# Kernel tuning notes

Measured on AMD Instinct MI355X. Metric: run time of the kernel, lower is better.

Reference implementation:

```python
import jax, jax.numpy as jnp
import numpy as np
from jax.scipy.special import gammaln, logsumexp

NEG = -1e9  # finite large-negative to keep gradients NaN-free


def setup_inputs() -> dict:
    key = jax.random.key(0)
    ks = jax.random.split(key, 8)
    B, T, D, C, K = 8, 4096, 64, 32, 20
    features = jax.random.normal(ks[0], (B, T, D), dtype=jnp.float32)
    # valid lengths in [T//2, T] so every sequence is long relative to K
    lengths = jax.random.randint(ks[1], (B,), T // 2, T + 1)
    poisson_log_rates = jax.random.normal(ks[2], (C,), dtype=jnp.float32) * 0.1 + jnp.log(8.0)
    gaussian_means = jax.random.normal(ks[3], (C, D), dtype=jnp.float32) * 0.5
    # tied diagonal covariance (as produced by initialize_gaussian / tied_diag)
    gaussian_cov = jnp.diag(jax.random.uniform(ks[4], (D,), minval=0.5, maxval=1.5))
    transition_logits = jax.random.normal(ks[5], (C, C), dtype=jnp.float32) * 0.1
    init_logits = jax.random.uniform(ks[6], (C,), dtype=jnp.float32)
    return dict(features=features, poisson_log_rates=poisson_log_rates,
                gaussian_means=gaussian_means, gaussian_cov=gaussian_cov,
                transition_logits=transition_logits, init_logits=init_logits,
                lengths=lengths, max_k=K)


def reference(features, poisson_log_rates, gaussian_means, gaussian_cov,
              transition_logits, init_logits, lengths, max_k):
    B, T, D = features.shape
    C = gaussian_means.shape[0]
    K = int(max_k)

    # ---- emission log-probs: tied full-covariance Gaussian per class -> (B,T,C)
    prec = jnp.linalg.inv(gaussian_cov)
    _, logdet = jnp.linalg.slogdet(gaussian_cov)
    xP = features @ prec                                        # (B,T,D)
    quad = jnp.einsum('btd,btd->bt', xP, features)              # x^T P x
    cross = jnp.einsum('btd,cd->btc', xP, gaussian_means)       # x^T P mu
    muPmu = jnp.einsum('cd,de,ce->c', gaussian_means, prec, gaussian_means)
    const = D * jnp.log(2.0 * jnp.pi) + logdet
    emit = -0.5 * (quad[:, :, None] - 2.0 * cross + muPmu[None, None, :] + const)  # (B,T,C)

    # ---- Poisson duration scores for d = 1..K -> (K,C)
    d = jnp.arange(1, K + 1, dtype=jnp.float32)[:, None]
    length_scores = d * poisson_log_rates[None, :] - jnp.exp(poisson_log_rates)[None, :] - gammaln(d + 1.0)

    # ---- normalized transition (to <- from, softmax over 'to' axis) and init
    trans = jax.nn.log_softmax(transition_logits, axis=0)       # trans[to, from]
    init = jax.nn.log_softmax(init_logits)

    # ---- span emission sums via cumsum differences (== sliding_sum windows)
    cum = jnp.concatenate([jnp.zeros((B, 1, C), emit.dtype), jnp.cumsum(emit, axis=1)], axis=1)  # (B,T+1,C)
    t_idx = jnp.arange(1, T + 1)[:, None]                        # (T,1) span end (exclusive)
    d_idx = jnp.arange(1, K + 1)[None, :]                        # (1,K) duration
    start = jnp.clip(t_idx - d_idx, 0, None)                     # (T,K) span start
    span = cum[:, t_idx, :] - cum[:, start, :]                   # (B,T,K,C)
    seg = span + length_scores[None, None, :, :]                 # add duration scores
    seg = jnp.transpose(seg, (1, 2, 0, 3))                       # (T,K,B,C)
    dur_valid = (d_idx <= t_idx)                                 # (T,K): need d <= t
    seg = jnp.where(dur_valid[:, :, None, None], seg, NEG)

    # ---- semi-Markov forward recursion over time.
    # buf[i] = alpha_star[t-1-i]; alpha_star[s][c] = best-sum of paths ending a
    # segment at s, already including the transition into the next label c.
    buf0 = jnp.full((K, B, C), NEG, emit.dtype).at[0].set(jnp.broadcast_to(init, (B, C)))

    def step(buf, seg_t):
        alpha_t = logsumexp(buf + seg_t, axis=0)                               # (B,C)
        astar = logsumexp(alpha_t[:, None, :] + trans[None, :, :], axis=2)     # (B,C)
        buf = jnp.concatenate([astar[None], buf[:-1]], axis=0)
        return buf, alpha_t

    _, alphas = jax.lax.scan(step, buf0, seg)                    # (T,B,C)
    logZ = logsumexp(alphas[lengths - 1, jnp.arange(B), :], axis=-1)
    return -logZ  # negative log marginal likelihood per sequence
```

## Files before the change

### kernel.cpp

```cpp
#include <hip/hip_runtime.h>
#include <math.h>

#define TT 4096
#define DD 64
#define CC 32
#define KK 20
#define TP 4112
#define NEGV -1.0e9f
#define L2E 1.44269504088896340736f
#define LN2f 0.69314718055994530942f

#if __has_builtin(__builtin_amdgcn_permlane32_swap)
#define HAVE_PLSWAP 1
#endif
#if __has_builtin(__builtin_amdgcn_permlane16_swap)
#define HAVE_PL16 1
#endif

__device__ __align__(16) float g_pmu[32 * 64];
__device__ __align__(16) float g_p2[64];
__device__ __align__(16) float g_mc[32];
__device__ __align__(16) float g_ls2[20 * 32];
__device__ __align__(16) float g_T[32 * 32];
__device__ __align__(16) float g_init2[32];
__device__ float g_cum[8 * TT * CC];
__device__ __align__(16) float g_cumT[8 * 32 * TP];

__device__ __forceinline__ float fexp2(float x) {
#if __has_builtin(__builtin_amdgcn_exp2f)
    return __builtin_amdgcn_exp2f(x);
#else
    return __exp2f(x);
#endif
}
__device__ __forceinline__ float flog2(float x) {
#if __has_builtin(__builtin_amdgcn_logf)
    return __builtin_amdgcn_logf(x);
#else
    return __log2f(x);
#endif
}

#define RF(x) __int_as_float(__builtin_amdgcn_readfirstlane(__float_as_int(x)))

__device__ __forceinline__ float xswap32(float x) {
#ifdef HAVE_PLSWAP
    int xi = __float_as_int(x);
    auto pr = __builtin_amdgcn_permlane32_swap(xi, xi, false, false);
    int r0 = ((const int*)&pr)[0];
    int r1 = ((const int*)&pr)[1];
    return (r0 == xi) ? __int_as_float(r1) : __int_as_float(r0);
#else
    return __shfl_xor(x, 32);
#endif
}

__device__ __forceinline__ float xswap16(float x) {
#ifdef HAVE_PL16
    int xi = __float_as_int(x);
    auto pr = __builtin_amdgcn_permlane16_swap(xi, xi, false, false);
    int r0 = ((const int*)&pr)[0];
    int r1 = ((const int*)&pr)[1];
    return (r0 == xi) ? __int_as_float(r1) : __int_as_float(r0);
#else
    return __shfl_xor(x, 16);
#endif
}

#define DPPF(dst, src, CTRL) \
    dst = __int_as_float(__builtin_amdgcn_update_dpp(0, __float_as_int(src), (CTRL), 0xF, 0xF, 1))

__global__ void smm_setup(const float* __restrict__ plr,
                          const float* __restrict__ mu,
                          const float* __restrict__ cov,
                          const float* __restrict__ tl,
                          const float* __restrict__ il) {
    int l = threadIdx.x;
    __shared__ float red[64];
    __shared__ float constc_s;
    float cd = cov[l * 64 + l];
    float pd = 1.0f / cd;
    red[l] = logf(cd);
    __syncthreads();
    if (l == 0) {
        float s = 0.f;
        for (int i = 0; i < 64; ++i) s += red[i];
        constc_s = 64.0f * logf(2.0f * 3.14159265358979323846f) + s;
    }
    __syncthreads();
    float constc = constc_s;

    g_p2[l] = 0.5f * L2E * pd;
    for (int c2 = 0; c2 < 32; ++c2)
        g_pmu[c2 * 64 + l] = L2E * pd * mu[c2 * 64 + l];

    if (l < 32) {
        float s = 0.f;
        for (int d2 = 0; d2 < 64; ++d2) {
            float m_ = mu[l * 64 + d2];
            s += m_ * m_ / cov[d2 * 64 + d2];
        }
        g_mc[l] = -0.5f * L2E * (s + constc);
    }
    for (int idx = l; idx < KK * CC; idx += 64) {
        int k = idx >> 5, c2 = idx & 31;
        float lr = plr[c2];
        g_ls2[idx] = L2E * ((float)(k + 1) * lr - expf(lr) - lgammaf((float)(k + 2)));
    }
    if (l < 32) {
        int from = l;
        float mx = -1e30f;
        for (int to = 0; to < 32; ++to) mx = fmaxf(mx, tl[to * 32 + from]);
        float s = 0.f;
        for (int to = 0; to < 32; ++to) s += expf(tl[to * 32 + from] - mx);
        float inv = 1.0f / s;
        for (int to = 0; to < 32; ++to)
            g_T[to * 32 + from] = expf(tl[to * 32 + from] - mx) * inv;
    }
    if (l == 32) {
        float mx = -1e30f;
        for (int c2 = 0; c2 < 32; ++c2) mx = fmaxf(mx, il[c2]);
        float s = 0.f;
        for (int c2 = 0; c2 < 32; ++c2) s += expf(il[c2] - mx);
        float lse = mx + logf(s);
        for (int c2 = 0; c2 < 32; ++c2) g_init2[c2] = L2E * (il[c2] - lse);
    }
}

__global__ __launch_bounds__(256) void smm_emit(const float* __restrict__ feat) {
    int tid = threadIdx.x;
    int c = tid & 31, tl_ = tid >> 5;
    int t = blockIdx.x * 8 + tl_;
    int b = blockIdx.y;
    const float4* x4 = (const float4*)(feat + ((size_t)b * TT + t) * DD);
    const float4* pm4 = (const float4*)(g_pmu + c * 64);
    const float4* p24 = (const float4*)g_p2;
    float acc = g_mc[c];
#pragma unroll
    for (int i = 0; i < 16; ++i) {
        float4 xv = x4[i], pm = pm4[i], pv = p24[i];
        acc = fmaf(pm.x, xv.x, acc); acc = fmaf(-pv.x * xv.x, xv.x, acc);
        acc = fmaf(pm.y, xv.y, acc); acc = fmaf(-pv.y * xv.y, xv.y, acc);
        acc = fmaf(pm.z, xv.z, acc); acc = fmaf(-pv.z * xv.z, xv.z, acc);
        acc = fmaf(pm.w, xv.w, acc); acc = fmaf(-pv.w * xv.w, xv.w, acc);
    }
    g_cum[((size_t)b * TT + t) * CC + c] = acc;
}

__global__ __launch_bounds__(256) void smm_scan() {
    int b = blockIdx.x;
    int tid = threadIdx.x;
    int c = tid & 31, g = tid >> 5;
    float* base = g_cum + (size_t)b * TT * CC + c;
    float* outT = g_cumT + ((size_t)b * 32 + c) * TP;
    int t0 = g * 512;
    float run = 0.f;
    for (int t = t0; t < t0 + 512; t += 8) {
        float v[8];
#pragma unroll
        for (int j = 0; j < 8; ++j) v[j] = base[(size_t)(t + j) * CC];
#pragma unroll
        for (int j = 0; j < 8; ++j) { run += v[j]; base[(size_t)(t + j) * CC] = run; }
    }
    __shared__ float tot[8][32];
    tot[g][c] = run;
    __syncthreads();
    float pre = 0.f;
#pragma unroll
    for (int gg = 0; gg < 7; ++gg) if (gg < g) pre += tot[gg][c];
    for (int t = t0; t < t0 + 512; t += 8) {
        float v[8];
#pragma unroll
        for (int j = 0; j < 8; ++j) v[j] = base[(size_t)(t + j) * CC] + pre;
        float4 w0, w1;
        w0.x = v[0]; w0.y = v[1]; w0.z = v[2]; w0.w = v[3];
        w1.x = v[4]; w1.y = v[5]; w1.z = v[6]; w1.w = v[7];
        *(float4*)(outT + t) = w0;
        *(float4*)(outT + t + 4) = w1;
    }
}

#define STEP(CUMV, CUMNEXT, tcur)                                                \
    {                                                                            \
         \
        float pf = fmaf(accf, nu, OFF);                                          \
        float g1,g2,g3,g4,g5,g6,g7,g8,g9,g10,g11,g12,g13,g14,g15;                \
        DPPF(g1,  pf, 0xB1);                                                     \
        DPPF(g2,  pf, 0x4E);  DPPF(g3,  g1, 0x4E);                               \
        DPPF(g7,  pf, 0x141); DPPF(g6,  g1, 0x141);                              \
        DPPF(g5,  g2, 0x141); DPPF(g4,  g3, 0x141);                              \
        DPPF(g15, pf, 0x140); DPPF(g14, g1, 0x140);                              \
        DPPF(g13, g2, 0x140); DPPF(g12, g3, 0x140);                              \
        DPPF(g11, g4, 0x140); DPPF(g10, g5, 0x140);                              \
        DPPF(g9,  g6, 0x140); DPPF(g8,  g7, 0x140);                              \
        float a0 = Tr[0]*pf;   a0 = fmaf(Tr[1], g1, a0);  a0 = fmaf(Tr[2], g2, a0);  a0 = fmaf(Tr[3], g3, a0); \
        float a1 = Tr[4]*g4;   a1 = fmaf(Tr[5], g5, a1);  a1 = fmaf(Tr[6], g6, a1);  a1 = fmaf(Tr[7], g7, a1); \
        float a2 = Tr[8]*g8;   a2 = fmaf(Tr[9], g9, a2);  a2 = fmaf(Tr[10],g10,a2);  a2 = fmaf(Tr[11],g11,a2); \
        float a3 = Tr[12]*g12; a3 = fmaf(Tr[13],g13,a3);  a3 = fmaf(Tr[14],g14,a3);  a3 = fmaf(Tr[15],g15,a3); \
        float accl = (a0 + a1) + (a2 + a3);                                      \
        float p48  = xswap16(xswap32(accl));                                     \
        float naccf = fmaxf(accl + p48, 1e-30f);                                 \
                                         \
        pfL  = ((tcur) == lenm1) ? pf   : pfL;                                   \
        refL = ((tcur) == lenm1) ? refc : refL;                                  \
         \
        float aL   = rfc64p + flog2(fmaxf(RF(pfPrev), 1e-37f));                  \
        float rcN  = RF(CUMNEXT);                                                \
        float refn = aL + (rcN - rcPrev);                                        \
        float cKn  = (CUMNEXT - refn) - 64.0f;                                   \
        float sg   = fexp2(cKn - cK);                                            \
        float nun  = sg * E1;                                                    \
                \
        float u2   = accf * nu;                                                  \
        float s0   = half ? Wc : u2;                                             \
        float t9   = (q9 * rxr) * sg;                                            \
        float x9   = xswap32(t9);                                                \
        float Wn   = half ? x9 : t9;                                             \
        q9 = (q8*rho[8])*sg; q8 = (q7*rho[7])*sg; q7 = (q6*rho[6])*sg;           \
        q6 = (q5*rho[5])*sg; q5 = (q4*rho[4])*sg; q4 = (q3*rho[3])*sg;           \
        q3 = (q2*rho[2])*sg; q2 = (q1*rho[1])*sg; q1 = (s0*rho[0])*sg;           \
        float S = (((q1+q2)+(q3+q4)) + ((q5+q6)+(q7+q8))) + q9;                  \
        float OFFn = (S + xswap32(S)) + Wn;                                      \
                                           \
        rfc64p = refc + 64.0f;                                                   \
        rcPrev = RF(CUMV);                                                       \
        pfPrev = pf;                                                             \
        Wc = Wn; accf = naccf; nu = nun; OFF = OFFn; cK = cKn; refc = refn;      \
    }

__global__ __launch_bounds__(64, 1)
void smm_forward(const int* __restrict__ lens, float* __restrict__ out) {
    const int b = blockIdx.x;
    const int l = threadIdx.x;
    const int c = l & 31;
    const int half = l >> 5;
    const int i16 = l & 15;
    const int rb = ((l >> 4) & 1) * 16;
    const int cT = half ? (c ^ 16) : c;

    float lsr[10];
#pragma unroll
    for (int i = 0; i < 10; ++i) lsr[i] = g_ls2[(half * 10 + i) * 32 + c];

    float Tr[16];
#pragma unroll
    for (int j2 = 0; j2 < 16; ++j2) Tr[j2] = g_T[cT * 32 + rb + (i16 ^ j2)];

    float tswp = xswap32(lsr[0]);
    float ls1c = half ? tswp : lsr[0];
    float d11s = half ? lsr[0] : tswp;

    float rho[9];
#pragma unroll
    for (int i = 0; i < 9; ++i) rho[i] = fexp2(lsr[i + 1] - lsr[i]);
    float rxr = fexp2(d11s - lsr[9]);
    float E1  = fexp2(ls1c);

    int len = lens[b];
    if (len < 1) len = 1;
    if (len > TT) len = TT;
    const int lenm1 = len - 1;
    int nsteps = (len + 7) & ~7;

    const float* cumbT = g_cumT + ((size_t)b * 32 + c) * TP;
    const float4* cp = (const float4*)cumbT;
    float4 cA = cp[0], cB = cp[1], pA = cp[2], pB = cp[3];

    float q1=0.f,q2=0.f,q3=0.f,q4=0.f,q5=0.f,q6=0.f,q7=0.f,q8=0.f,q9=0.f;
    float Wc = 0.f;
    float iv   = g_init2[c] + ls1c;
    float refc = RF(cA.x + iv);
    float cK   = (cA.x - refc) - 64.0f;
    float nu   = fexp2(iv + cK);
    float accf = 1.0f, OFF = 0.0f;
    float rfc64p = refc + 64.0f;
    float pfPrev = 5.421010862427522e-20f;
    float rcPrev = RF(cA.x);
    float pfL = 0.0f, refL = 0.0f;

    for (int tb = 0; tb < nsteps; tb += 8) {
        int bi = tb >> 2;
        float4 nA = cp[bi + 4], nB = cp[bi + 5];
        STEP(cA.x, cA.y, tb + 0); STEP(cA.y, cA.z, tb + 1);
        STEP(cA.z, cA.w, tb + 2); STEP(cA.w, cB.x, tb + 3);
        STEP(cB.x, cB.y, tb + 4); STEP(cB.y, cB.z, tb + 5);
        STEP(cB.z, cB.w, tb + 6); STEP(cB.w, pA.x, tb + 7);
        cA = pA; cB = pB; pA = nA; pB = nB;
    }

    float alpha2 = refL + 64.0f + flog2(fmaxf(pfL, 1e-37f));
    float m2 = alpha2, s2 = 1.0f;
#pragma unroll
    for (int st = 1; st < 32; st <<= 1) {
        float om = __shfl_xor(m2, st), os = __shfl_xor(s2, st);
        float M = fmaxf(m2, om);
        s2 = s2 * fexp2(m2 - M) + os * fexp2(om - M);
        m2 = M;
    }
    if (l == 0) out[b] = -LN2f * (m2 + flog2(s2));
}

extern "C" void kernel_launch(void* const* d_in, const int* in_sizes, int n_in,
                              void* d_out, int out_size, void* d_ws, size_t ws_size,
                              hipStream_t stream) {
    const float* feat = (const float*)d_in[0];
    const float* plr  = (const float*)d_in[1];
    const float* mu   = (const float*)d_in[2];
    const float* cov  = (const float*)d_in[3];
    const float* tl   = (const float*)d_in[4];
    const float* il   = (const float*)d_in[5];
    const int*   lens = (const int*)d_in[6];
    float* outf = (float*)d_out;
    int B = in_sizes[6];
    if (B > 8) B = 8;

    smm_setup<<<1, 64, 0, stream>>>(plr, mu, cov, tl, il);
    smm_emit<<<dim3(TT / 8, B), 256, 0, stream>>>(feat);
    smm_scan<<<B, 256, 0, stream>>>();
    smm_forward<<<B, 64, 0, stream>>>(lens, outf);
}
```

Baseline: 829.0 us.

## Replace cumulative-sum scan with per-step exponentiated emissions and periodic rescaling

Drops the separate prefix-scan kernel. The emit kernel now writes exp2 of the emission minus a global bias, already transposed, and the forward recursion multiplies these factors directly instead of differencing cumulative sums. Renormalisation happens every four steps through a feedback controller that accumulates a double-precision reference offset. The DPP shuffle tree is also restructured. The goal is to cut a kernel launch and per-step log/exp work, at the cost of more delicate numerical stability.

```diff
diff --git a/kernel.cpp b/kernel.cpp
--- a/kernel.cpp
+++ b/kernel.cpp
@@ -5,10 +5,10 @@
 #define DD 64
 #define CC 32
 #define KK 20
-#define TP 4112
-#define NEGV -1.0e9f
+#define TPE 4128
 #define L2E 1.44269504088896340736f
 #define LN2f 0.69314718055994530942f
+#define PIN 20.0f
 
 #if __has_builtin(__builtin_amdgcn_permlane32_swap)
 #define HAVE_PLSWAP 1
@@ -23,8 +23,8 @@
 __device__ __align__(16) float g_ls2[20 * 32];
 __device__ __align__(16) float g_T[32 * 32];
 __device__ __align__(16) float g_init2[32];
-__device__ float g_cum[8 * TT * CC];
-__device__ __align__(16) float g_cumT[8 * 32 * TP];
+__device__ float g_mb;
+__device__ __align__(16) float g_eT[8 * 32 * TPE];
 
 __device__ __forceinline__ float fexp2(float x) {
 #if __has_builtin(__builtin_amdgcn_exp2f)
@@ -77,10 +77,13 @@
                           const float* __restrict__ il) {
     int l = threadIdx.x;
     __shared__ float red[64];
+    __shared__ float redp[64];
+    __shared__ float muP[32];
     __shared__ float constc_s;
     float cd = cov[l * 64 + l];
     float pd = 1.0f / cd;
     red[l] = logf(cd);
+    redp[l] = pd;
     __syncthreads();
     if (l == 0) {
         float s = 0.f;
@@ -101,6 +104,7 @@
             s += m_ * m_ / cov[d2 * 64 + d2];
         }
         g_mc[l] = -0.5f * L2E * (s + constc);
+        muP[l] = s;
     }
     for (int idx = l; idx < KK * CC; idx += 64) {
         int k = idx >> 5, c2 = idx & 31;
@@ -124,6 +128,15 @@
         for (int c2 = 0; c2 < 32; ++c2) s += expf(il[c2] - mx);
         float lse = mx + logf(s);
         for (int c2 = 0; c2 < 32; ++c2) g_init2[c2] = L2E * (il[c2] - lse);
+    }
+    __syncthreads();
+    if (l == 0) {
+        float trP = 0.f;
+        for (int i = 0; i < 64; ++i) trP += redp[i];
+        float mm = 0.f;
+        for (int c2 = 0; c2 < 32; ++c2) mm += muP[c2];
+        mm *= (1.0f / 32.0f);
+        g_mb = -0.5f * L2E * (constc + trP + mm);
     }
 }
 
@@ -144,88 +157,70 @@
         acc = fmaf(pm.z, xv.z, acc); acc = fmaf(-pv.z * xv.z, xv.z, acc);
         acc = fmaf(pm.w, xv.w, acc); acc = fmaf(-pv.w * xv.w, xv.w, acc);
     }
-    g_cum[((size_t)b * TT + t) * CC + c] = acc;
-}
-
-__global__ __launch_bounds__(256) void smm_scan() {
-    int b = blockIdx.x;
-    int tid = threadIdx.x;
-    int c = tid & 31, g = tid >> 5;
-    float* base = g_cum + (size_t)b * TT * CC + c;
-    float* outT = g_cumT + ((size_t)b * 32 + c) * TP;
-    int t0 = g * 512;
-    float run = 0.f;
-    for (int t = t0; t < t0 + 512; t += 8) {
-        float v[8];
-#pragma unroll
-        for (int j = 0; j < 8; ++j) v[j] = base[(size_t)(t + j) * CC];
-#pragma unroll
-        for (int j = 0; j < 8; ++j) { run += v[j]; base[(size_t)(t + j) * CC] = run; }
-    }
-    __shared__ float tot[8][32];
-    tot[g][c] = run;
+    float ev = fexp2(acc - g_mb);
+    __shared__ float stage[32][9];
+    stage[c][tl_] = ev;
     __syncthreads();
-    float pre = 0.f;
-#pragma unroll
-    for (int gg = 0; gg < 7; ++gg) if (gg < g) pre += tot[gg][c];
-    for (int t = t0; t < t0 + 512; t += 8) {
-        float v[8];
-#pragma unroll
-        for (int j = 0; j < 8; ++j) v[j] = base[(size_t)(t + j) * CC] + pre;
-        float4 w0, w1;
-        w0.x = v[0]; w0.y = v[1]; w0.z = v[2]; w0.w = v[3];
-        w1.x = v[4]; w1.y = v[5]; w1.z = v[6]; w1.w = v[7];
-        *(float4*)(outT + t) = w0;
-        *(float4*)(outT + t + 4) = w1;
-    }
-}
-
-#define STEP(CUMV, CUMNEXT, tcur)                                                \
-    {                                                                            \
-         \
-        float pf = fmaf(accf, nu, OFF);                                          \
-        float g1,g2,g3,g4,g5,g6,g7,g8,g9,g10,g11,g12,g13,g14,g15;                \
-        DPPF(g1,  pf, 0xB1);                                                     \
-        DPPF(g2,  pf, 0x4E);  DPPF(g3,  g1, 0x4E);                               \
-        DPPF(g7,  pf, 0x141); DPPF(g6,  g1, 0x141);                              \
-        DPPF(g5,  g2, 0x141); DPPF(g4,  g3, 0x141);                              \
-        DPPF(g15, pf, 0x140); DPPF(g14, g1, 0x140);                              \
-        DPPF(g13, g2, 0x140); DPPF(g12, g3, 0x140);                              \
-        DPPF(g11, g4, 0x140); DPPF(g10, g5, 0x140);                              \
-        DPPF(g9,  g6, 0x140); DPPF(g8,  g7, 0x140);                              \
-        float a0 = Tr[0]*pf;   a0 = fmaf(Tr[1], g1, a0);  a0 = fmaf(Tr[2], g2, a0);  a0 = fmaf(Tr[3], g3, a0); \
-        float a1 = Tr[4]*g4;   a1 = fmaf(Tr[5], g5, a1);  a1 = fmaf(Tr[6], g6, a1);  a1 = fmaf(Tr[7], g7, a1); \
-        float a2 = Tr[8]*g8;   a2 = fmaf(Tr[9], g9, a2);  a2 = fmaf(Tr[10],g10,a2);  a2 = fmaf(Tr[11],g11,a2); \
-        float a3 = Tr[12]*g12; a3 = fmaf(Tr[13],g13,a3);  a3 = fmaf(Tr[14],g14,a3);  a3 = fmaf(Tr[15],g15,a3); \
-        float accl = (a0 + a1) + (a2 + a3);                                      \
-        float p48  = xswap16(xswap32(accl));                                     \
-        float naccf = fmaxf(accl + p48, 1e-30f);                                 \
-                                         \
-        pfL  = ((tcur) == lenm1) ? pf   : pfL;                                   \
-        refL = ((tcur) == lenm1) ? refc : refL;                                  \
-         \
-        float aL   = rfc64p + flog2(fmaxf(RF(pfPrev), 1e-37f));                  \
-        float rcN  = RF(CUMNEXT);                                                \
-        float refn = aL + (rcN - rcPrev);                                        \
-        float cKn  = (CUMNEXT - refn) - 64.0f;                                   \
-        float sg   = fexp2(cKn - cK);                                            \
-        float nun  = sg * E1;                                                    \
-                \
-        float u2   = accf * nu;                                                  \
-        float s0   = half ? Wc : u2;                                             \
-        float t9   = (q9 * rxr) * sg;                                            \
-        float x9   = xswap32(t9);                                                \
-        float Wn   = half ? x9 : t9;                                             \
-        q9 = (q8*rho[8])*sg; q8 = (q7*rho[7])*sg; q7 = (q6*rho[6])*sg;           \
-        q6 = (q5*rho[5])*sg; q5 = (q4*rho[4])*sg; q4 = (q3*rho[3])*sg;           \
-        q3 = (q2*rho[2])*sg; q2 = (q1*rho[1])*sg; q1 = (s0*rho[0])*sg;           \
-        float S = (((q1+q2)+(q3+q4)) + ((q5+q6)+(q7+q8))) + q9;                  \
-        float OFFn = (S + xswap32(S)) + Wn;                                      \
-                                           \
-        rfc64p = refc + 64.0f;                                                   \
-        rcPrev = RF(CUMV);                                                       \
-        pfPrev = pf;                                                             \
-        Wc = Wn; accf = naccf; nu = nun; OFF = OFFn; cK = cKn; refc = refn;      \
+    int c2 = tid >> 3, j = tid & 7;
+    int t0 = blockIdx.x * 8;
+    int ti = (t0 + j + TT - 1) & (TT - 1);
+    g_eT[((size_t)b * 32 + c2) * TPE + ti] = stage[c2][j];
+}
+
+#define STEP(EV, tcur)                                                            \
+    {                                                                             \
+        float pf = fmaf(accf, nu, OFF);                                           \
+        float G1, G2, G3, G7, G15;                                                \
+        DPPF(G1, pf, 0xB1); DPPF(G2, pf, 0x4E); DPPF(G3, pf, 0x1B);               \
+        DPPF(G7, pf, 0x141); DPPF(G15, pf, 0x140);                                \
+        float G4, G5, G6, G8, G12, G13, G14;                                      \
+        DPPF(G6, G1, 0x141); DPPF(G5, G2, 0x141); DPPF(G4, G3, 0x141);            \
+        DPPF(G8, G7, 0x140); DPPF(G14, G1, 0x140); DPPF(G13, G2, 0x140);          \
+        DPPF(G12, G3, 0x140);                                                     \
+        float G9, G10, G11;                                                       \
+        DPPF(G9, G14, 0x141); DPPF(G10, G13, 0x141); DPPF(G11, G12, 0x141);       \
+        float a0 = Tr[0]*pf;   a0 = fmaf(Tr[1],G1,a0);   a0 = fmaf(Tr[2],G2,a0);   a0 = fmaf(Tr[3],G3,a0);    \
+        float a1 = Tr[4]*G4;   a1 = fmaf(Tr[5],G5,a1);   a1 = fmaf(Tr[6],G6,a1);   a1 = fmaf(Tr[7],G7,a1);    \
+        float a2 = Tr[8]*G8;   a2 = fmaf(Tr[9],G9,a2);   a2 = fmaf(Tr[10],G10,a2); a2 = fmaf(Tr[11],G11,a2);  \
+        float a3 = Tr[12]*G12; a3 = fmaf(Tr[13],G13,a3); a3 = fmaf(Tr[14],G14,a3); a3 = fmaf(Tr[15],G15,a3);  \
+        float accl = (a0 + a1) + (a2 + a3);                                       \
+        float p48 = xswap16(xswap32(accl));                                       \
+        float naccf = accl + p48;                                                 \
+        pfc = pf;                                                                 \
+        if ((tcur) == lenm1) { pfL = pf; refL = refc; }                           \
+        float sg = (EV) * su;                                                     \
+        float u2 = accf * nu;                                                     \
+        float s0 = half ? Wc : u2;                                                \
+        float e9 = z9 * sg;                                                       \
+        float t9 = e9 * rr;                                                       \
+        float x9 = xswap32(t9);                                                   \
+        float Wn = half ? x9 : t9;                                                \
+        z9 = z8*sg; z8 = z7*sg; z7 = z6*sg; z6 = z5*sg; z5 = z4*sg;               \
+        z4 = z3*sg; z3 = z2*sg; z2 = z1*sg; z1 = s0*sg;                           \
+        float tA = Pw1*z1; tA = fmaf(Pw2,z2,tA); tA = fmaf(Pw3,z3,tA);            \
+        tA = fmaf(Pw4,z4,tA); tA = fmaf(Pw5,z5,tA);                               \
+        float tB = Pw6*z6; tB = fmaf(Pw7,z7,tB); tB = fmaf(Pw8,z8,tB);            \
+        tB = fmaf(Pw9,z9,tB);                                                     \
+        float S = tA + tB;                                                        \
+        float Sx = xswap32(S);                                                    \
+        OFF = fmaxf((S + Sx) + Wn, 1e-36f);                                       \
+        nu = sg * E1;                                                             \
+        accf = naccf;                                                             \
+        Wc = Wn;                                                                  \
+        refc += (double)r8;                                                       \
+    }
+
+#define CTRLDB(gain)                                                              \
+    {                                                                             \
+        float err = flog2(fmaxf(RF(pfc), 1e-37f)) + PIN;                          \
+        err = fminf(fmaxf(err, -40.0f), 40.0f);                                   \
+        float cs = fexp2(-err);                                                   \
+        accf *= cs; OFF *= cs; Wc *= cs;                                          \
+        z1*=cs; z2*=cs; z3*=cs; z4*=cs; z5*=cs;                                   \
+        z6*=cs; z7*=cs; z8*=cs; z9*=cs;                                           \
+        refc += (double)err;                                                      \
+        r8 = fmaf(err, (gain), r8);                                               \
+        su = fexp2(mb - r8);                                                      \
     }
 
 __global__ __launch_bounds__(64, 1)
@@ -246,14 +241,16 @@
 #pragma unroll
     for (int j2 = 0; j2 < 16; ++j2) Tr[j2] = g_T[cT * 32 + rb + (i16 ^ j2)];
 
-    float tswp = xswap32(lsr[0]);
+    float tswp = __shfl_xor(lsr[0], 32);
     float ls1c = half ? tswp : lsr[0];
     float d11s = half ? lsr[0] : tswp;
 
-    float rho[9];
-#pragma unroll
-    for (int i = 0; i < 9; ++i) rho[i] = fexp2(lsr[i + 1] - lsr[i]);
-    float rxr = fexp2(d11s - lsr[9]);
+    float Pw1 = fexp2(lsr[1] - lsr[0]), Pw2 = fexp2(lsr[2] - lsr[0]);
+    float Pw3 = fexp2(lsr[3] - lsr[0]), Pw4 = fexp2(lsr[4] - lsr[0]);
+    float Pw5 = fexp2(lsr[5] - lsr[0]), Pw6 = fexp2(lsr[6] - lsr[0]);
+    float Pw7 = fexp2(lsr[7] - lsr[0]), Pw8 = fexp2(lsr[8] - lsr[0]);
+    float Pw9 = fexp2(lsr[9] - lsr[0]);
+    float rr  = fexp2(d11s - lsr[0]);
     float E1  = fexp2(ls1c);
 
     int len = lens[b];
@@ -262,42 +259,51 @@
     const int lenm1 = len - 1;
     int nsteps = (len + 7) & ~7;
 
-    const float* cumbT = g_cumT + ((size_t)b * 32 + c) * TP;
-    const float4* cp = (const float4*)cumbT;
+    const float* eT = g_eT + ((size_t)b * 32 + c) * TPE;
+    const float4* cp = (const float4*)eT;
     float4 cA = cp[0], cB = cp[1], pA = cp[2], pB = cp[3];
 
-    float q1=0.f,q2=0.f,q3=0.f,q4=0.f,q5=0.f,q6=0.f,q7=0.f,q8=0.f,q9=0.f;
+    float mb = g_mb;
+    float e0 = eT[TT - 1];
+    float iv = g_init2[c] + ls1c;
+    float a0v = iv + mb + flog2(fmaxf(e0, 1e-37f));
+    float refc0 = RF(a0v);
+    double refc = (double)refc0;
+    float nu = e0 * fexp2(iv + mb - refc0 - PIN);
+    float accf = 1.0f, OFF = 0.0f;
+    float z1=0.f,z2=0.f,z3=0.f,z4=0.f,z5=0.f,z6=0.f,z7=0.f,z8=0.f,z9=0.f;
     float Wc = 0.f;
-    float iv   = g_init2[c] + ls1c;
-    float refc = RF(cA.x + iv);
-    float cK   = (cA.x - refc) - 64.0f;
-    float nu   = fexp2(iv + cK);
-    float accf = 1.0f, OFF = 0.0f;
-    float rfc64p = refc + 64.0f;
-    float pfPrev = 5.421010862427522e-20f;
-    float rcPrev = RF(cA.x);
-    float pfL = 0.0f, refL = 0.0f;
-
-    for (int tb = 0; tb < nsteps; tb += 8) {
+    float r8 = mb;
+    float su = 1.0f;
+    float pfL = 0.f, pfc = 0.f;
+    double refL = 0.0;
+
+    {
+        float4 nA = cp[4], nB = cp[5];
+        STEP(cA.x, 0); CTRLDB(0.3f); STEP(cA.y, 1); CTRLDB(0.3f);
+        STEP(cA.z, 2); CTRLDB(0.3f); STEP(cA.w, 3); CTRLDB(0.3f);
+        STEP(cB.x, 4); CTRLDB(0.3f); STEP(cB.y, 5); CTRLDB(0.3f);
+        STEP(cB.z, 6); CTRLDB(0.3f); STEP(cB.w, 7); CTRLDB(0.3f);
+        cA = pA; cB = pB; pA = nA; pB = nB;
+    }
+
+    for (int tb = 8; tb < nsteps; tb += 8) {
         int bi = tb >> 2;
         float4 nA = cp[bi + 4], nB = cp[bi + 5];
-        STEP(cA.x, cA.y, tb + 0); STEP(cA.y, cA.z, tb + 1);
-        STEP(cA.z, cA.w, tb + 2); STEP(cA.w, cB.x, tb + 3);
-        STEP(cB.x, cB.y, tb + 4); STEP(cB.y, cB.z, tb + 5);
-        STEP(cB.z, cB.w, tb + 6); STEP(cB.w, pA.x, tb + 7);
+        STEP(cA.x, tb + 0); STEP(cA.y, tb + 1); STEP(cA.z, tb + 2); STEP(cA.w, tb + 3);
+        CTRLDB(0.125f);
+        STEP(cB.x, tb + 4); STEP(cB.y, tb + 5); STEP(cB.z, tb + 6); STEP(cB.w, tb + 7);
+        CTRLDB(0.125f);
         cA = pA; cB = pB; pA = nA; pB = nB;
     }
 
-    float alpha2 = refL + 64.0f + flog2(fmaxf(pfL, 1e-37f));
-    float m2 = alpha2, s2 = 1.0f;
+    float tot = pfL;
 #pragma unroll
-    for (int st = 1; st < 32; st <<= 1) {
-        float om = __shfl_xor(m2, st), os = __shfl_xor(s2, st);
-        float M = fmaxf(m2, om);
-        s2 = s2 * fexp2(m2 - M) + os * fexp2(om - M);
-        m2 = M;
-    }
-    if (l == 0) out[b] = -LN2f * (m2 + flog2(s2));
+    for (int st = 1; st < 32; st <<= 1) tot += __shfl_xor(tot, st);
+    if (l == 0) {
+        double a = refL + (double)PIN + (double)flog2(fmaxf(tot, 1e-37f));
+        out[b] = (float)(-0.69314718055994530942 * a);
+    }
 }
 
 extern "C" void kernel_launch(void* const* d_in, const int* in_sizes, int n_in,
@@ -316,6 +322,5 @@
 
     smm_setup<<<1, 64, 0, stream>>>(plr, mu, cov, tl, il);
     smm_emit<<<dim3(TT / 8, B), 256, 0, stream>>>(feat);
-    smm_scan<<<B, 256, 0, stream>>>();
     smm_forward<<<B, 64, 0, stream>>>(lens, outf);
 }
```

After: 680.3 us. 1.22x faster.
